# Optimization experiments

Measured on AMD Instinct MI355X. Metric: run time of the kernel, lower is better.

Reference implementation:

```python
import jax, jax.numpy as jnp
import numpy as np

N_NODES = 100000
BN_EPS = 1e-5


def gcn_conv(x, src, dst, W, b, n):
    # PyG GCNConv: add self-loops, symmetric norm D^-1/2 (A+I) D^-1/2, then linear.
    h = x @ W                                   # [N, F_out]
    deg = jnp.zeros((n,), h.dtype).at[dst].add(1.0)   # in-degree incl. self-loops
    dinv = jnp.where(deg > 0, jax.lax.rsqrt(deg), 0.0)
    norm = dinv[src] * dinv[dst]                # [E+N]
    msg = h[src] * norm[:, None]                # gather + scale, [E+N, F_out]
    out = jax.ops.segment_sum(msg, dst, num_segments=n)
    return out + b


def setup_inputs() -> dict:
    key = jax.random.key(0)
    ks = jax.random.split(key, 6)
    N, E, F_in, H, C = N_NODES, 1600000, 128, 64, 64
    x = jax.random.normal(ks[0], (N, F_in), dtype=jnp.float32)
    edge_index = jax.random.randint(ks[1], (2, E), 0, N, dtype=jnp.int64)
    W1 = jax.random.normal(ks[2], (F_in, H), dtype=jnp.float32) * (1.0 / np.sqrt(F_in))
    b1 = jnp.zeros((H,), jnp.float32)
    W2 = jax.random.normal(ks[3], (H, C), dtype=jnp.float32) * (1.0 / np.sqrt(H))
    b2 = jnp.zeros((C,), jnp.float32)
    gamma = jnp.ones((H,), jnp.float32)
    beta = jnp.zeros((H,), jnp.float32)
    return {"x": x, "edge_index": edge_index, "W1": W1, "b1": b1,
            "W2": W2, "b2": b2, "gamma": gamma, "beta": beta}


def reference(x, edge_index, W1, b1, W2, b2, gamma, beta):
    n = x.shape[0]
    loop = jnp.arange(n, dtype=edge_index.dtype)
    src = jnp.concatenate([edge_index[0], loop])
    dst = jnp.concatenate([edge_index[1], loop])
    # dropout(p=0.8) acts as identity in eval mode (deterministic baseline)
    h = gcn_conv(x, src, dst, W1, b1, n)
    # BatchNorm1d with batch statistics (biased var), as in training-mode math
    mean = jnp.mean(h, axis=0)
    var = jnp.mean(jnp.square(h - mean), axis=0)
    h = (h - mean) * jax.lax.rsqrt(var + BN_EPS) * gamma + beta
    h = jax.nn.relu(h)
    out = gcn_conv(h, src, dst, W2, b2, n)
    return out
```

## Files before the change

kernel.cpp:

```cpp
#include <hip/hip_runtime.h>

#define BN_EPS 1e-5f
#define SCAN_CHUNK 2048
#define EPB 16384
#define NBUCK 512

__device__ __forceinline__ float bf2f(unsigned short u) {
  return __uint_as_float(((unsigned)u) << 16);
}
__device__ __forceinline__ unsigned short f2bf(float f) {
  unsigned b = __float_as_uint(f);
  b += 0x7FFFu + ((b >> 16) & 1u);
  return (unsigned short)(b >> 16);
}

template<int K, bool FUSE_BN, bool SCALE>
__device__ __forceinline__ void gemm_tile(float* __restrict__ Xs,
                                          float* __restrict__ bn_s, int tile,
                                          const float* __restrict__ X,
                                          const float* __restrict__ W,
                                          const float* __restrict__ dinv,
                                          const float* __restrict__ stats,
                                          const float* __restrict__ gamma,
                                          const float* __restrict__ beta,
                                          unsigned short* __restrict__ Y,
                                          int n, float inv_n) {
  constexpr int XS = K + 4;
  const int t = threadIdx.x;
  const int base = tile * 64;
  float* mean_s = bn_s;
  float* scl_s  = bn_s + 64;
  float* bt_s   = bn_s + 128;

  if (FUSE_BN) {
    if (t < 64) {
      float mean = stats[t] * inv_n;
      float var = stats[64 + t] * inv_n - mean * mean;
      mean_s[t] = mean;
      scl_s[t] = rsqrtf(var + BN_EPS) * gamma[t];
      bt_s[t] = beta[t];
    }
    __syncthreads();
  }

  {
    constexpr int RV = K / 4;
    for (int idx = t; idx < 64 * RV; idx += 256) {
      int row = idx / RV, kk = idx % RV;
      float4 v = make_float4(0.f, 0.f, 0.f, 0.f);
      if (base + row < n) {
        v = *(const float4*)(X + (size_t)(base + row) * K + kk * 4);
        if (FUSE_BN) {
          int k0 = kk * 4;
          v.x = fmaxf(fmaf(v.x - mean_s[k0 + 0], scl_s[k0 + 0], bt_s[k0 + 0]), 0.f);
          v.y = fmaxf(fmaf(v.y - mean_s[k0 + 1], scl_s[k0 + 1], bt_s[k0 + 1]), 0.f);
          v.z = fmaxf(fmaf(v.z - mean_s[k0 + 2], scl_s[k0 + 2], bt_s[k0 + 2]), 0.f);
          v.w = fmaxf(fmaf(v.w - mean_s[k0 + 3], scl_s[k0 + 3], bt_s[k0 + 3]), 0.f);
        }
      }
      *(float4*)(Xs + row * XS + kk * 4) = v;
    }
  }
  __syncthreads();

  const int tc = t & 15;
  const int tr = t >> 4;
  const float* wp = W + tc * 4;

  float acc[4][4];
#pragma unroll
  for (int r = 0; r < 4; ++r)
#pragma unroll
    for (int c = 0; c < 4; ++c) acc[r][c] = 0.f;

  float4 wc[4], wn[4];
#pragma unroll
  for (int kk = 0; kk < 4; ++kk) wc[kk] = *(const float4*)(wp + kk * 64);

#pragma unroll 4
  for (int k = 0; k < K; k += 4) {
    float4 xr[4];
#pragma unroll
    for (int r = 0; r < 4; ++r) xr[r] = *(const float4*)(Xs + (tr * 4 + r) * XS + k);
    if (k + 4 < K) {
#pragma unroll
      for (int kk = 0; kk < 4; ++kk) wn[kk] = *(const float4*)(wp + (k + 4 + kk) * 64);
    }
#pragma unroll
    for (int kk = 0; kk < 4; ++kk) {
#pragma unroll
      for (int r = 0; r < 4; ++r) {
        float xv = (kk == 0) ? xr[r].x : (kk == 1) ? xr[r].y : (kk == 2) ? xr[r].z : xr[r].w;
        acc[r][0] = fmaf(xv, wc[kk].x, acc[r][0]);
        acc[r][1] = fmaf(xv, wc[kk].y, acc[r][1]);
        acc[r][2] = fmaf(xv, wc[kk].z, acc[r][2]);
        acc[r][3] = fmaf(xv, wc[kk].w, acc[r][3]);
      }
    }
    if (k + 4 < K) {
#pragma unroll
      for (int kk = 0; kk < 4; ++kk) wc[kk] = wn[kk];
    }
  }

#pragma unroll
  for (int r = 0; r < 4; ++r) {
    int i = base + tr * 4 + r;
    if (i < n) {
      float sc = SCALE ? dinv[i] : 1.0f;
      ushort4 o;
      o.x = f2bf(acc[r][0] * sc);
      o.y = f2bf(acc[r][1] * sc);
      o.z = f2bf(acc[r][2] * sc);
      o.w = f2bf(acc[r][3] * sc);
      *(ushort4*)(Y + (size_t)i * 64 + tc * 4) = o;
    }
  }
}

__global__ __launch_bounds__(256) void k_fused_hist_gemm1(
    const int* __restrict__ dst, int* __restrict__ bh, int E, int nba,
    const float* __restrict__ X, const float* __restrict__ W,
    unsigned short* __restrict__ Y, int n, int nbT) {
  __shared__ float Xs[64 * 132];

  int paired = 2 * (nba < nbT ? nba : nbT);
  int role, idx;
  if ((int)blockIdx.x < paired) {
    role = blockIdx.x & 1;
    idx = blockIdx.x >> 1;
  } else {
    int r = blockIdx.x - paired;
    if (nba > nbT) { role = 0; idx = nbT + r; }
    else           { role = 1; idx = nba + r; }
  }

  if (role == 0) {
    int* hist = (int*)Xs;
    const int t = threadIdx.x;
    for (int b = t; b < NBUCK; b += 256) hist[b] = 0;
    __syncthreads();
    int ebase = idx * EPB;
#pragma unroll
    for (int i = 0; i < EPB / 1024; ++i) {
      int e = ebase + (i * 256 + t) * 4;
      if (e + 3 < E) {
        int4 d4 = *(const int4*)(dst + e);
        atomicAdd(&hist[d4.x >> 8], 1);
        atomicAdd(&hist[d4.y >> 8], 1);
        atomicAdd(&hist[d4.z >> 8], 1);
        atomicAdd(&hist[d4.w >> 8], 1);
      } else {
        for (int q = e; q < E && q < e + 4; ++q) atomicAdd(&hist[dst[q] >> 8], 1);
      }
    }
    __syncthreads();
    for (int b = t; b < NBUCK; b += 256) bh[(size_t)b * nba + idx] = hist[b];
    return;
  }
  gemm_tile<128, false, false>(Xs, nullptr, idx, X, W,
                               nullptr, nullptr, nullptr, nullptr, Y, n, 0.f);
}

__global__ __launch_bounds__(256) void k_bscan_local(int* __restrict__ a,
                                                     int* __restrict__ bsum, int M) {
  __shared__ int ts[256];
  int base = blockIdx.x * SCAN_CHUNK;
  int t = threadIdx.x;
  int idx0 = base + t * 8;
  int v[8];
  int s = 0;
#pragma unroll
  for (int k = 0; k < 8; ++k) {
    int i = idx0 + k;
    int d = (i < M) ? a[i] : 0;
    v[k] = s;
    s += d;
  }
  int val = s;
  ts[t] = val;
  __syncthreads();
#pragma unroll
  for (int off = 1; off < 256; off <<= 1) {
    int add = (t >= off) ? ts[t - off] : 0;
    __syncthreads();
    val += add;
    ts[t] = val;
    __syncthreads();
  }
  int excl = val - s;
#pragma unroll
  for (int k = 0; k < 8; ++k) {
    int i = idx0 + k;
    if (i < M) a[i] = excl + v[k];
  }
  if (t == 255) bsum[blockIdx.x] = val;
}

__global__ void k_bscan_blk(int* __restrict__ bsum, int nblk) {
  if (threadIdx.x == 0) {
    int run = 0;
    for (int i = 0; i < nblk; ++i) { int v = bsum[i]; bsum[i] = run; run += v; }
  }
}

__global__ __launch_bounds__(256) void k_bscan_add(int* __restrict__ a,
                                                   const int* __restrict__ bsum, int M) {
  int off = bsum[blockIdx.x];
  int base = blockIdx.x * SCAN_CHUNK;
  for (int k = threadIdx.x; k < SCAN_CHUNK; k += 256) {
    int i = base + k;
    if (i < M) a[i] += off;
  }
}

__global__ __launch_bounds__(256) void k_scatter(
    const int* __restrict__ src, const int* __restrict__ dst,
    const int* __restrict__ bh, int* __restrict__ sval, int E, int nba) {
  __shared__ int cur[NBUCK];
  const int t = threadIdx.x;
  for (int b = t; b < NBUCK; b += 256) cur[b] = bh[(size_t)b * nba + blockIdx.x];
  __syncthreads();
  int ebase = blockIdx.x * EPB;
#pragma unroll
  for (int i = 0; i < EPB / 1024; ++i) {
    int e = ebase + (i * 256 + t) * 4;
    if (e + 3 < E) {
      int4 d4 = *(const int4*)(dst + e);
      int4 s4 = *(const int4*)(src + e);
      int p0 = atomicAdd(&cur[d4.x >> 8], 1);
      int p1 = atomicAdd(&cur[d4.y >> 8], 1);
      int p2 = atomicAdd(&cur[d4.z >> 8], 1);
      int p3 = atomicAdd(&cur[d4.w >> 8], 1);
      sval[p0] = s4.x | ((d4.x & 255) << 20);
      sval[p1] = s4.y | ((d4.y & 255) << 20);
      sval[p2] = s4.z | ((d4.z & 255) << 20);
      sval[p3] = s4.w | ((d4.w & 255) << 20);
    } else {
      for (int q = e; q < E && q < e + 4; ++q) {
        int d = dst[q];
        int p = atomicAdd(&cur[d >> 8], 1);
        sval[p] = src[q] | ((d & 255) << 20);
      }
    }
  }
}

__global__ __launch_bounds__(256) void k_group_deg(
    const int* __restrict__ sval, const int* __restrict__ bh,
    int* __restrict__ deg, int nba, int n) {
  __shared__ int cnt[256];
  const int t = threadIdx.x;
  const int b = blockIdx.x;
  cnt[t] = 0;
  __syncthreads();
  int lo = bh[(size_t)b * nba];
  int end = bh[(size_t)(b + 1) * nba];
  for (int i = lo + t; i < end; i += 256)
    atomicAdd(&cnt[(sval[i] >> 20) & 255], 1);
  __syncthreads();
  int node = b * 256 + t;
  if (node < n) deg[node] = cnt[t];
}


__global__ __launch_bounds__(256) void k_scan_local(const int* __restrict__ deg,
                                                    int* __restrict__ row_ptr,
                                                    int* __restrict__ blksum,
                                                    float* __restrict__ dinv, int n) {
  __shared__ int ts[256];
  int base = blockIdx.x * SCAN_CHUNK;
  int t = threadIdx.x;
  int idx0 = base + t * 8;
  int v[8];
  int s = 0;
#pragma unroll
  for (int k = 0; k < 8; ++k) {
    int i = idx0 + k;
    int d = (i < n) ? deg[i] : 0;
    if (i < n) dinv[i] = rsqrtf(1.0f + (float)d);
    v[k] = s;
    s += d;
  }
  int val = s;
  ts[t] = val;
  __syncthreads();
#pragma unroll
  for (int off = 1; off < 256; off <<= 1) {
    int add = (t >= off) ? ts[t - off] : 0;
    __syncthreads();
    val += add;
    ts[t] = val;
    __syncthreads();
  }
  int excl = val - s;
#pragma unroll
  for (int k = 0; k < 8; ++k) {
    int i = idx0 + k;
    if (i < n) row_ptr[i] = excl + v[k];
  }
  if (t == 255) blksum[blockIdx.x] = val;
}

__global__ void k_scan_blk(int* __restrict__ blksum, int nblk,
                           int* __restrict__ row_ptr, int n,
                           float* __restrict__ stats) {
  for (int i = threadIdx.x; i < 128; i += 64) stats[i] = 0.f;
  if (threadIdx.x == 0) {
    int run = 0;
    for (int i = 0; i < nblk; ++i) { int v = blksum[i]; blksum[i] = run; run += v; }
    row_ptr[n] = run;
  }
}

__global__ __launch_bounds__(256) void k_scan_add(int* __restrict__ row_ptr,
                                                  const int* __restrict__ blksum, int n) {
  int off = blksum[blockIdx.x];
  int base = blockIdx.x * SCAN_CHUNK;
  for (int k = threadIdx.x; k < SCAN_CHUNK; k += 256) {
    int i = base + k;
    if (i < n) row_ptr[i] += off;
  }
}

__global__ __launch_bounds__(256) void k_fused_fill_scale(
    const int* __restrict__ sval, const int* __restrict__ bh,
    const int* __restrict__ row_ptr, int* __restrict__ col, int nba, int nbu,
    unsigned short* __restrict__ h16, const float* __restrict__ dinv, int n) {
  __shared__ int cur[256];
  const int t = threadIdx.x;
  if ((int)blockIdx.x < nbu) {
    const int b = blockIdx.x;
    int node = b * 256 + t;
    cur[t] = (node < n) ? row_ptr[node] : 0;
    __syncthreads();
    int lo = bh[(size_t)b * nba];
    int end = bh[(size_t)(b + 1) * nba];
    for (int i = lo + t; i < end; i += 256) {
      int v = sval[i];
      int p = atomicAdd(&cur[(v >> 20) & 255], 1);
      col[p] = v & 0x1FFFF;
    }
    return;
  }
  int si = blockIdx.x - nbu;
  int idx = (si * 256 + t) * 8;
  if (idx >= n * 64) return;
  int row = idx >> 6;
  float di = dinv[row];
  uint4 v = *(const uint4*)(h16 + idx);
  unsigned r[4] = {v.x, v.y, v.z, v.w};
#pragma unroll
  for (int q = 0; q < 4; ++q) {
    float lo = bf2f((unsigned short)(r[q] & 0xFFFFu)) * di;
    float hi = bf2f((unsigned short)(r[q] >> 16)) * di;
    r[q] = ((unsigned)f2bf(hi) << 16) | f2bf(lo);
  }
  *(uint4*)(h16 + idx) = make_uint4(r[0], r[1], r[2], r[3]);
}

__global__ __launch_bounds__(256) void k_gather_p(
    const unsigned short* __restrict__ Hs,
    const int* __restrict__ row_ptr,
    const int* __restrict__ col,
    const float* __restrict__ dinv,
    const float* __restrict__ b,
    float* __restrict__ out, int n) {
  const uint2* H64 = (const uint2*)Hs;
  int lane = threadIdx.x & 63;
  int wv = threadIdx.x >> 6;
  int i = blockIdx.x * 4 + wv;
  if (i >= n) return;
  int quarter = lane >> 4;
  int q = lane & 15;
  int p0 = row_ptr[i], p1 = row_ptr[i + 1];
  int nl = p1 - p0;
  int L = nl + 1;
  int cl = (lane == 0) ? i : ((lane <= nl) ? col[p0 + lane - 1] : i);
  int Lc = (L < 32) ? L : 32;
  bool two = (Lc > 16);

  uint2 u[8];
  float ww[8];
#pragma unroll
  for (int s = 0; s < 4; ++s) {
    int vidx = quarter * 4 + s;
    int vc = (vidx < Lc) ? vidx : 0;
    int c = __shfl(cl, vc);
    u[s] = H64[(size_t)c * 16 + q];
    ww[s] = (vidx < Lc) ? 1.0f : 0.0f;
  }
  if (two) {
#pragma unroll
    for (int s = 4; s < 8; ++s) {
      int vidx = 16 + quarter * 4 + (s - 4);
      int vc = (vidx < Lc) ? vidx : 0;
      int c = __shfl(cl, vc);
      u[s] = H64[(size_t)c * 16 + q];
      ww[s] = (vidx < Lc) ? 1.0f : 0.0f;
    }
  }

  float a0 = 0.f, a1 = 0.f, a2 = 0.f, a3 = 0.f;
#pragma unroll
  for (int s = 0; s < 4; ++s) {
    a0 = fmaf(ww[s], bf2f((unsigned short)u[s].x), a0);
    a1 = fmaf(ww[s], bf2f((unsigned short)(u[s].x >> 16)), a1);
    a2 = fmaf(ww[s], bf2f((unsigned short)u[s].y), a2);
    a3 = fmaf(ww[s], bf2f((unsigned short)(u[s].y >> 16)), a3);
  }
  if (two) {
#pragma unroll
    for (int s = 4; s < 8; ++s) {
      a0 = fmaf(ww[s], bf2f((unsigned short)u[s].x), a0);
      a1 = fmaf(ww[s], bf2f((unsigned short)(u[s].x >> 16)), a1);
      a2 = fmaf(ww[s], bf2f((unsigned short)u[s].y), a2);
      a3 = fmaf(ww[s], bf2f((unsigned short)(u[s].y >> 16)), a3);
    }
  }
  for (int v = 32 + quarter; v < L; v += 4) {
    int c = col[p0 + v - 1];
    uint2 uu = H64[(size_t)c * 16 + q];
    a0 += bf2f((unsigned short)uu.x);
    a1 += bf2f((unsigned short)(uu.x >> 16));
    a2 += bf2f((unsigned short)uu.y);
    a3 += bf2f((unsigned short)(uu.y >> 16));
  }
  a0 += __shfl_down(a0, 16); a0 += __shfl_down(a0, 32);
  a1 += __shfl_down(a1, 16); a1 += __shfl_down(a1, 32);
  a2 += __shfl_down(a2, 16); a2 += __shfl_down(a2, 32);
  a3 += __shfl_down(a3, 16); a3 += __shfl_down(a3, 32);
  if (lane < 16) {
    float di = dinv[i];
    float4 bb = *(const float4*)(b + 4 * q);
    float4 o;
    o.x = fmaf(di, a0, bb.x);
    o.y = fmaf(di, a1, bb.y);
    o.z = fmaf(di, a2, bb.z);
    o.w = fmaf(di, a3, bb.w);
    *(float4*)(out + (size_t)i * 64 + 4 * q) = o;
  }
}

__global__ __launch_bounds__(256) void k_bnstats(const float* __restrict__ A,
                                                 float* __restrict__ stats, int n) {
  int j = threadIdx.x & 63;
  int r = threadIdx.x >> 6;
  float s = 0.f, s2 = 0.f;
  for (int i = blockIdx.x * 4 + r; i < n; i += gridDim.x * 4) {
    float v = A[(size_t)i * 64 + j];
    s += v;
    s2 += v * v;
  }
  __shared__ float ls[256], ls2[256];
  ls[threadIdx.x] = s;
  ls2[threadIdx.x] = s2;
  __syncthreads();
  if (threadIdx.x < 64) {
    atomicAdd(&stats[j], ls[j] + ls[j + 64] + ls[j + 128] + ls[j + 192]);
    atomicAdd(&stats[64 + j], ls2[j] + ls2[j + 64] + ls2[j + 128] + ls2[j + 192]);
  }
}

__global__ __launch_bounds__(256) void k_gemm2(const float* __restrict__ X,
                                               const float* __restrict__ W,
                                               const float* __restrict__ dinv,
                                               const float* __restrict__ stats,
                                               const float* __restrict__ gamma,
                                               const float* __restrict__ beta,
                                               unsigned short* __restrict__ Y,
                                               int n, float inv_n) {
  __shared__ float Xs[64 * 68];
  __shared__ float bn_s[192];
  gemm_tile<64, true, true>(Xs, bn_s, blockIdx.x, X, W, dinv, stats, gamma, beta,
                            Y, n, inv_n);
}


extern "C" void kernel_launch(void* const* d_in, const int* in_sizes, int n_in,
                              void* d_out, int out_size, void* d_ws, size_t ws_size,
                              hipStream_t stream) {
  const float* x     = (const float*)d_in[0];
  const int*   ei    = (const int*)d_in[1];
  const float* W1    = (const float*)d_in[2];
  const float* b1    = (const float*)d_in[3];
  const float* W2    = (const float*)d_in[4];
  const float* b2    = (const float*)d_in[5];
  const float* gamma = (const float*)d_in[6];
  const float* beta  = (const float*)d_in[7];
  float* out = (float*)d_out;

  const int N = in_sizes[0] / 128;
  const int E = in_sizes[1] / 2;
  const int* src = ei;
  const int* dst = ei + E;

  const size_t Npad = ((size_t)N + 256) & ~(size_t)255;

  char* p = (char*)d_ws;
  float* dinv    = (float*)p;               p += Npad * 4;
  int*   deg     = (int*)p;                 p += Npad * 4;
  int*   row_ptr = (int*)p;                 p += Npad * 4;
  int*   blksum  = (int*)p;                 p += 256 * 4;
  int*   sval    = (int*)p;                 p += (size_t)E * 4;
  int*   col     = (int*)p;                 p += (size_t)E * 4;
  unsigned short* h16 = (unsigned short*)p; p += (size_t)N * 64 * 2;
  float* agg     = (float*)p;               p += (size_t)N * 64 * 4;
  float* stats   = (float*)p;               p += 128 * 4;

  int* bh = (int*)agg;

  int nb_n4 = (N + 3) / 4;
  int nb_t  = (N + 63) / 64;
  int nba   = (E + EPB - 1) / EPB;
  int nbu   = (N + 255) / 256;
  int nbS   = (N * 64 + 2047) / 2048;
  int nscan = (N + SCAN_CHUNK - 1) / SCAN_CHUNK;
  int M     = NBUCK * nba;
  int nbM   = (M + SCAN_CHUNK - 1) / SCAN_CHUNK;
  float inv_n = 1.0f / (float)N;

  k_fused_hist_gemm1<<<nba + nb_t, 256, 0, stream>>>(dst, bh, E, nba,
                                                     x, W1, h16, N, nb_t);

  k_bscan_local<<<nbM, 256, 0, stream>>>(bh, blksum, M);
  k_bscan_blk<<<1, 64, 0, stream>>>(blksum, nbM);
  k_bscan_add<<<nbM, 256, 0, stream>>>(bh, blksum, M);
  k_scatter<<<nba, 256, 0, stream>>>(src, dst, bh, sval, E, nba);

  k_group_deg<<<nbu, 256, 0, stream>>>(sval, bh, deg, nba, N);

  k_scan_local<<<nscan, 256, 0, stream>>>(deg, row_ptr, blksum, dinv, N);
  k_scan_blk<<<1, 64, 0, stream>>>(blksum, nscan, row_ptr, N, stats);
  k_scan_add<<<nscan, 256, 0, stream>>>(row_ptr, blksum, N);

  k_fused_fill_scale<<<nbu + nbS, 256, 0, stream>>>(sval, bh, row_ptr, col,
                                                    nba, nbu, h16, dinv, N);

  k_gather_p<<<nb_n4, 256, 0, stream>>>(h16, row_ptr, col, dinv, b1, agg, N);

  k_bnstats<<<1024, 256, 0, stream>>>(agg, stats, N);

  k_gemm2<<<nb_t, 256, 0, stream>>>(agg, W2, dinv, stats, gamma, beta, h16, N, inv_n);
  k_gather_p<<<nb_n4, 256, 0, stream>>>(h16, row_ptr, col, dinv, b2, out, N);
}
```

Before: 337.6 us.

## Make both GEMMs persistent with LDS-resident weights and register-prefetched X tiles

Both dense GEMMs now run as persistent grids of 512 blocks that stride over 64-row tiles. Each block copies the full weight matrix into shared memory once and software-pipelines the next tile's X rows through registers while computing the current tile. This removes the repeated global weight loads per tile and hides X load latency. In exchange shared memory per block grows (up to about 66KB for GEMM1), which lowers occupancy, and the interleaved histogram/GEMM block pairing in the fused kernel is dropped.

```diff
diff --git a/kernel.cpp b/kernel.cpp
--- a/kernel.cpp
+++ b/kernel.cpp
@@ -4,6 +4,7 @@
 #define SCAN_CHUNK 2048
 #define EPB 16384
 #define NBUCK 512
+#define NBG 512
 
 __device__ __forceinline__ float bf2f(unsigned short u) {
   return __uint_as_float(((unsigned)u) << 16);
@@ -15,129 +16,162 @@
 }
 
 template<int K, bool FUSE_BN, bool SCALE>
-__device__ __forceinline__ void gemm_tile(float* __restrict__ Xs,
-                                          float* __restrict__ bn_s, int tile,
-                                          const float* __restrict__ X,
-                                          const float* __restrict__ W,
-                                          const float* __restrict__ dinv,
-                                          const float* __restrict__ stats,
-                                          const float* __restrict__ gamma,
-                                          const float* __restrict__ beta,
-                                          unsigned short* __restrict__ Y,
-                                          int n, float inv_n) {
+__device__ __forceinline__ void gemm_persist(
+    float* __restrict__ Ws, float* __restrict__ Xs, float* __restrict__ bn_s,
+    int tile0, int stride, int nT,
+    const float* __restrict__ X, const float* __restrict__ W,
+    const float* __restrict__ dinv, const float* __restrict__ stats,
+    const float* __restrict__ gamma, const float* __restrict__ beta,
+    unsigned short* __restrict__ Y, int n, float inv_n) {
   constexpr int XS = K + 4;
+  constexpr int RV = K / 4;
+  constexpr int NL = (64 * RV) / 256;
   const int t = threadIdx.x;
-  const int base = tile * 64;
-  float* mean_s = bn_s;
-  float* scl_s  = bn_s + 64;
-  float* bt_s   = bn_s + 128;
 
   if (FUSE_BN) {
     if (t < 64) {
       float mean = stats[t] * inv_n;
       float var = stats[64 + t] * inv_n - mean * mean;
-      mean_s[t] = mean;
-      scl_s[t] = rsqrtf(var + BN_EPS) * gamma[t];
-      bt_s[t] = beta[t];
-    }
-    __syncthreads();
-  }
-
+      bn_s[t] = mean;
+      bn_s[64 + t] = rsqrtf(var + BN_EPS) * gamma[t];
+      bn_s[128 + t] = beta[t];
+    }
+  }
   {
-    constexpr int RV = K / 4;
-    for (int idx = t; idx < 64 * RV; idx += 256) {
+    const float4* wv = (const float4*)W;
+    float4* wsv = (float4*)Ws;
+    for (int idx = t; idx < K * 16; idx += 256) wsv[idx] = wv[idx];
+  }
+
+  const int tc = t & 15;
+  const int tr = t >> 4;
+
+  float4 xg[NL];
+  int tile = tile0;
+  {
+    int base = tile * 64;
+#pragma unroll
+    for (int j = 0; j < NL; ++j) {
+      int idx = t + j * 256;
       int row = idx / RV, kk = idx % RV;
       float4 v = make_float4(0.f, 0.f, 0.f, 0.f);
-      if (base + row < n) {
-        v = *(const float4*)(X + (size_t)(base + row) * K + kk * 4);
-        if (FUSE_BN) {
+      if (base + row < n) v = *(const float4*)(X + (size_t)(base + row) * K + kk * 4);
+      xg[j] = v;
+    }
+  }
+  __syncthreads();
+  {
+    int base = tile * 64;
+#pragma unroll
+    for (int j = 0; j < NL; ++j) {
+      int idx = t + j * 256;
+      int row = idx / RV, kk = idx % RV;
+      float4 v = xg[j];
+      if (FUSE_BN && base + row < n) {
+        int k0 = kk * 4;
+        v.x = fmaxf(fmaf(v.x - bn_s[k0 + 0], bn_s[64 + k0 + 0], bn_s[128 + k0 + 0]), 0.f);
+        v.y = fmaxf(fmaf(v.y - bn_s[k0 + 1], bn_s[64 + k0 + 1], bn_s[128 + k0 + 1]), 0.f);
+        v.z = fmaxf(fmaf(v.z - bn_s[k0 + 2], bn_s[64 + k0 + 2], bn_s[128 + k0 + 2]), 0.f);
+        v.w = fmaxf(fmaf(v.w - bn_s[k0 + 3], bn_s[64 + k0 + 3], bn_s[128 + k0 + 3]), 0.f);
+      }
+      *(float4*)(Xs + row * XS + kk * 4) = v;
+    }
+  }
+  __syncthreads();
+
+  for (;;) {
+    const int next = tile + stride;
+    const bool havenext = (next < nT);
+    if (havenext) {
+      int nb2 = next * 64;
+#pragma unroll
+      for (int j = 0; j < NL; ++j) {
+        int idx = t + j * 256;
+        int row = idx / RV, kk = idx % RV;
+        float4 v = make_float4(0.f, 0.f, 0.f, 0.f);
+        if (nb2 + row < n) v = *(const float4*)(X + (size_t)(nb2 + row) * K + kk * 4);
+        xg[j] = v;
+      }
+    }
+
+    float acc[4][4];
+#pragma unroll
+    for (int r = 0; r < 4; ++r)
+#pragma unroll
+      for (int c = 0; c < 4; ++c) acc[r][c] = 0.f;
+
+#pragma unroll 4
+    for (int k = 0; k < K; k += 4) {
+      float4 xr[4], wr[4];
+#pragma unroll
+      for (int r = 0; r < 4; ++r) xr[r] = *(const float4*)(Xs + (tr * 4 + r) * XS + k);
+#pragma unroll
+      for (int kk = 0; kk < 4; ++kk) wr[kk] = *(const float4*)(Ws + (k + kk) * 64 + tc * 4);
+#pragma unroll
+      for (int kk = 0; kk < 4; ++kk) {
+#pragma unroll
+        for (int r = 0; r < 4; ++r) {
+          float xv = (kk == 0) ? xr[r].x : (kk == 1) ? xr[r].y : (kk == 2) ? xr[r].z : xr[r].w;
+          acc[r][0] = fmaf(xv, wr[kk].x, acc[r][0]);
+          acc[r][1] = fmaf(xv, wr[kk].y, acc[r][1]);
+          acc[r][2] = fmaf(xv, wr[kk].z, acc[r][2]);
+          acc[r][3] = fmaf(xv, wr[kk].w, acc[r][3]);
+        }
+      }
+    }
+
+    {
+      int base = tile * 64;
+#pragma unroll
+      for (int r = 0; r < 4; ++r) {
+        int i = base + tr * 4 + r;
+        if (i < n) {
+          float sc = SCALE ? dinv[i] : 1.0f;
+          ushort4 o;
+          o.x = f2bf(acc[r][0] * sc);
+          o.y = f2bf(acc[r][1] * sc);
+          o.z = f2bf(acc[r][2] * sc);
+          o.w = f2bf(acc[r][3] * sc);
+          *(ushort4*)(Y + (size_t)i * 64 + tc * 4) = o;
+        }
+      }
+    }
+
+    if (!havenext) break;
+    __syncthreads();
+    {
+      int nb2 = next * 64;
+#pragma unroll
+      for (int j = 0; j < NL; ++j) {
+        int idx = t + j * 256;
+        int row = idx / RV, kk = idx % RV;
+        float4 v = xg[j];
+        if (FUSE_BN && nb2 + row < n) {
           int k0 = kk * 4;
-          v.x = fmaxf(fmaf(v.x - mean_s[k0 + 0], scl_s[k0 + 0], bt_s[k0 + 0]), 0.f);
-          v.y = fmaxf(fmaf(v.y - mean_s[k0 + 1], scl_s[k0 + 1], bt_s[k0 + 1]), 0.f);
-          v.z = fmaxf(fmaf(v.z - mean_s[k0 + 2], scl_s[k0 + 2], bt_s[k0 + 2]), 0.f);
-          v.w = fmaxf(fmaf(v.w - mean_s[k0 + 3], scl_s[k0 + 3], bt_s[k0 + 3]), 0.f);
+          v.x = fmaxf(fmaf(v.x - bn_s[k0 + 0], bn_s[64 + k0 + 0], bn_s[128 + k0 + 0]), 0.f);
+          v.y = fmaxf(fmaf(v.y - bn_s[k0 + 1], bn_s[64 + k0 + 1], bn_s[128 + k0 + 1]), 0.f);
+          v.z = fmaxf(fmaf(v.z - bn_s[k0 + 2], bn_s[64 + k0 + 2], bn_s[128 + k0 + 2]), 0.f);
+          v.w = fmaxf(fmaf(v.w - bn_s[k0 + 3], bn_s[64 + k0 + 3], bn_s[128 + k0 + 3]), 0.f);
         }
-      }
-      *(float4*)(Xs + row * XS + kk * 4) = v;
-    }
-  }
-  __syncthreads();
-
-  const int tc = t & 15;
-  const int tr = t >> 4;
-  const float* wp = W + tc * 4;
-
-  float acc[4][4];
-#pragma unroll
-  for (int r = 0; r < 4; ++r)
-#pragma unroll
-    for (int c = 0; c < 4; ++c) acc[r][c] = 0.f;
-
-  float4 wc[4], wn[4];
-#pragma unroll
-  for (int kk = 0; kk < 4; ++kk) wc[kk] = *(const float4*)(wp + kk * 64);
-
-#pragma unroll 4
-  for (int k = 0; k < K; k += 4) {
-    float4 xr[4];
-#pragma unroll
-    for (int r = 0; r < 4; ++r) xr[r] = *(const float4*)(Xs + (tr * 4 + r) * XS + k);
-    if (k + 4 < K) {
-#pragma unroll
-      for (int kk = 0; kk < 4; ++kk) wn[kk] = *(const float4*)(wp + (k + 4 + kk) * 64);
-    }
-#pragma unroll
-    for (int kk = 0; kk < 4; ++kk) {
-#pragma unroll
-      for (int r = 0; r < 4; ++r) {
-        float xv = (kk == 0) ? xr[r].x : (kk == 1) ? xr[r].y : (kk == 2) ? xr[r].z : xr[r].w;
-        acc[r][0] = fmaf(xv, wc[kk].x, acc[r][0]);
-        acc[r][1] = fmaf(xv, wc[kk].y, acc[r][1]);
-        acc[r][2] = fmaf(xv, wc[kk].z, acc[r][2]);
-        acc[r][3] = fmaf(xv, wc[kk].w, acc[r][3]);
-      }
-    }
-    if (k + 4 < K) {
-#pragma unroll
-      for (int kk = 0; kk < 4; ++kk) wc[kk] = wn[kk];
-    }
-  }
-
-#pragma unroll
-  for (int r = 0; r < 4; ++r) {
-    int i = base + tr * 4 + r;
-    if (i < n) {
-      float sc = SCALE ? dinv[i] : 1.0f;
-      ushort4 o;
-      o.x = f2bf(acc[r][0] * sc);
-      o.y = f2bf(acc[r][1] * sc);
-      o.z = f2bf(acc[r][2] * sc);
-      o.w = f2bf(acc[r][3] * sc);
-      *(ushort4*)(Y + (size_t)i * 64 + tc * 4) = o;
-    }
+        *(float4*)(Xs + row * XS + kk * 4) = v;
+      }
+    }
+    __syncthreads();
+    tile = next;
   }
 }
 
 __global__ __launch_bounds__(256) void k_fused_hist_gemm1(
     const int* __restrict__ dst, int* __restrict__ bh, int E, int nba,
     const float* __restrict__ X, const float* __restrict__ W,
-    unsigned short* __restrict__ Y, int n, int nbT) {
+    unsigned short* __restrict__ Y, int n, int nT) {
+  __shared__ float Ws[128 * 64];
   __shared__ float Xs[64 * 132];
 
-  int paired = 2 * (nba < nbT ? nba : nbT);
-  int role, idx;
-  if ((int)blockIdx.x < paired) {
-    role = blockIdx.x & 1;
-    idx = blockIdx.x >> 1;
-  } else {
-    int r = blockIdx.x - paired;
-    if (nba > nbT) { role = 0; idx = nbT + r; }
-    else           { role = 1; idx = nba + r; }
-  }
-
-  if (role == 0) {
+  if ((int)blockIdx.x < nba) {
     int* hist = (int*)Xs;
     const int t = threadIdx.x;
+    const int idx = blockIdx.x;
     for (int b = t; b < NBUCK; b += 256) hist[b] = 0;
     __syncthreads();
     int ebase = idx * EPB;
@@ -158,8 +192,11 @@
     for (int b = t; b < NBUCK; b += 256) bh[(size_t)b * nba + idx] = hist[b];
     return;
   }
-  gemm_tile<128, false, false>(Xs, nullptr, idx, X, W,
-                               nullptr, nullptr, nullptr, nullptr, Y, n, 0.f);
+  int pid = blockIdx.x - nba;
+  int stride = gridDim.x - nba;
+  gemm_persist<128, false, false>(Ws, Xs, nullptr, pid, stride, nT,
+                                  X, W, nullptr, nullptr, nullptr, nullptr,
+                                  Y, n, 0.f);
 }
 
 __global__ __launch_bounds__(256) void k_bscan_local(int* __restrict__ a,
@@ -469,11 +506,12 @@
                                                const float* __restrict__ gamma,
                                                const float* __restrict__ beta,
                                                unsigned short* __restrict__ Y,
-                                               int n, float inv_n) {
+                                               int n, float inv_n, int nT) {
+  __shared__ float Ws[64 * 64];
   __shared__ float Xs[64 * 68];
   __shared__ float bn_s[192];
-  gemm_tile<64, true, true>(Xs, bn_s, blockIdx.x, X, W, dinv, stats, gamma, beta,
-                            Y, n, inv_n);
+  gemm_persist<64, true, true>(Ws, Xs, bn_s, blockIdx.x, gridDim.x, nT,
+                               X, W, dinv, stats, gamma, beta, Y, n, inv_n);
 }
 
 
@@ -520,8 +558,8 @@
   int nbM   = (M + SCAN_CHUNK - 1) / SCAN_CHUNK;
   float inv_n = 1.0f / (float)N;
 
-  k_fused_hist_gemm1<<<nba + nb_t, 256, 0, stream>>>(dst, bh, E, nba,
-                                                     x, W1, h16, N, nb_t);
+  k_fused_hist_gemm1<<<nba + NBG, 256, 0, stream>>>(dst, bh, E, nba,
+                                                    x, W1, h16, N, nb_t);
 
   k_bscan_local<<<nbM, 256, 0, stream>>>(bh, blksum, M);
   k_bscan_blk<<<1, 64, 0, stream>>>(blksum, nbM);
@@ -541,6 +579,7 @@
 
   k_bnstats<<<1024, 256, 0, stream>>>(agg, stats, N);
 
-  k_gemm2<<<nb_t, 256, 0, stream>>>(agg, W2, dinv, stats, gamma, beta, h16, N, inv_n);
+  k_gemm2<<<NBG, 256, 0, stream>>>(agg, W2, dinv, stats, gamma, beta, h16, N,
+                                   inv_n, nb_t);
   k_gather_p<<<nb_n4, 256, 0, stream>>>(h16, row_ptr, col, dinv, b2, out, N);
 }
```

Measured after the change: 327.4 us. 1.03x faster.
